# Performance work log

Hardware: AMD Instinct MI355X
Metric: run time of the kernel (lower is better)

The kernel has to match this reference:

```python
import jax, jax.numpy as jnp
import numpy as np
import math

NP2 = 64      # number of RF pulses
V = 32768     # number of voxels


def _shift_matrix(kmax):
    """EPG shift matrix, exact translation of EPG_shift_matrices."""
    N = 3 * (kmax + 1)
    S = np.zeros(N * N, dtype=np.complex64)
    kidx = list(range(3, N, 3)); sidx = [x - 3 for x in kidx]
    S[[a + N * b for a, b in zip(kidx, sidx)]] = 1
    kidx = list(range(4, N, 3)); kidx.pop(); sidx = [x + 3 for x in kidx]
    S[[a + N * b for a, b in zip(kidx, sidx)]] = 1
    kidx = list(range(2, N, 3))
    S[[a + N * b for a, b in zip(kidx, kidx)]] = 1
    S = S.reshape(N, N).T.copy()
    S[0:2, 4] = 1
    return jnp.asarray(S, dtype=jnp.complex64)


def _rf_rot_all(theta):
    """RF rotation matrices for all pulses at once. theta: [P] complex -> [P,3,3]."""
    a = jnp.abs(theta)
    phi = jnp.angle(theta)
    ca2 = (jnp.cos(a / 2) ** 2).astype(jnp.complex64)
    sa2 = jnp.sin(a / 2) ** 2
    sa = jnp.sin(a)
    ca = jnp.cos(a).astype(jnp.complex64)
    ep = jnp.exp(1j * phi)
    em = jnp.exp(-1j * phi)
    e2m = jnp.exp(-2j * phi)
    r00 = ca2
    r10 = e2m * sa2
    r20 = -0.5j * em * sa
    r01 = jnp.conj(r10)
    r11 = ca2
    r21 = 0.5j * ep * sa
    r02 = -1j * ep * sa
    r12 = 1j * em * sa
    r22 = ca
    row0 = jnp.stack([r00, r01, r02], axis=-1)
    row1 = jnp.stack([r10, r11, r12], axis=-1)
    row2 = jnp.stack([r20, r21, r22], axis=-1)
    return jnp.stack([row0, row1, row2], axis=-2).astype(jnp.complex64)


def _epg_gre_f0(theta, T1, T2, TR):
    """Single-compartment GRE EPG recurrence. Returns F0 signal [V, np2].

    Uses full-width (kmax) state updates every pulse: states beyond
    kmax_per_pulse are exactly zero on the ramp-up and cannot influence
    F0 on the ramp-down, so F0 matches the variable-width torch loop.
    """
    np2 = theta.shape[0]
    kmax = np2 - 1
    kpp_max = math.ceil(np2 / 2)
    if kpp_max < kmax:
        kmax = kpp_max
    K = kmax + 1
    N = 3 * K
    v = T1.shape[0]

    St = _shift_matrix(kmax).T                      # [N,N], so S @ f == f @ St
    E1 = jnp.exp(-TR / T1)[:, 0]                    # [V]
    E2 = jnp.exp(-TR / T2)[:, 0]                    # [V]
    # diagonal of kron(I_K, diag(E2,E2,E1)) per voxel -> [V,N]
    e = jnp.tile(jnp.stack([E2, E2, E1], axis=1), (1, K)).astype(jnp.complex64)
    b = jnp.zeros((v, N), jnp.complex64).at[:, 2].set((1 - E1).astype(jnp.complex64))

    A_all = _rf_rot_all(theta)                      # [np2,3,3]
    FF0 = jnp.zeros((v, N), jnp.complex64).at[:, 2].set(1.0)

    def step(FF, A):
        # block-diag kron(I_K, A) applied to the state vector
        Fcol = jnp.einsum('ab,vkb->vka', A, FF.reshape(v, K, 3)).reshape(v, N)
        # relaxation * shift + recovery
        FFn = e * (Fcol @ St) + b
        FFn = FFn.at[:, 0].set(jnp.conj(FFn[:, 0]))
        return FFn, Fcol[:, 0]

    _, F0 = jax.lax.scan(step, FF0, A_all)          # F0: [np2, V]
    return F0.T                                     # [V, np2]


def setup_inputs() -> dict:
    key = jax.random.key(0)
    k1, k2, k3, k4, k5 = jax.random.split(key, 5)
    flip = jax.random.uniform(k1, (NP2,), minval=0.1, maxval=math.pi / 2)
    phase = jax.random.uniform(k2, (NP2,), minval=-math.pi, maxval=math.pi)
    theta_re = (flip * jnp.cos(phase)).astype(jnp.float32)
    theta_im = (flip * jnp.sin(phase)).astype(jnp.float32)
    PD = jax.random.uniform(k3, (V, 1), minval=0.2, maxval=1.0)
    T1 = jax.random.uniform(k4, (V, 1), minval=300.0, maxval=1500.0)
    T2 = jax.random.uniform(k5, (V, 1), minval=20.0, maxval=120.0)
    qmaps = jnp.stack([PD, T1, T2], axis=0).astype(jnp.float32)  # [3,V,1]
    TR = jnp.array([10.0], jnp.float32)
    return {"theta_re": theta_re, "theta_im": theta_im, "TR": TR,
            "quantitative_maps": qmaps}


def reference(theta_re, theta_im, TR, quantitative_maps):
    theta = (theta_re + 1j * theta_im).astype(jnp.complex64)
    PD = quantitative_maps[0]   # [V,1]
    T1 = quantitative_maps[1]   # [V,1]
    T2 = quantitative_maps[2]   # [V,1]
    s = _epg_gre_f0(theta, T1, T2, TR)   # [V, np2] complex
    return jnp.abs(s) * PD
```

## Files before the change

### kernel.cpp

```cpp
#include <hip/hip_runtime.h>
#include <math.h>


#define NP2 64
#define ROR1  0x121
#define ROR15 0x12F

typedef float v2f __attribute__((ext_vector_type(2)));
typedef float v8f __attribute__((ext_vector_type(8)));

template<int CTRL>
__device__ __forceinline__ float rowrot(float x) {
    return __int_as_float(
        __builtin_amdgcn_mov_dpp(__float_as_int(x), CTRL, 0xF, 0xF, true));
}
__device__ __forceinline__ v2f mk2(float a, float b) { v2f r; r.x = a; r.y = b; return r; }

#define PAIR(V, i)  __builtin_shufflevector((V), (V), (i), (i) + 1)
#define FMA2(a, b, c) __builtin_elementwise_fma((a), (b), (c))

__global__ void coef_kernel(const float* __restrict__ theta_re,
                            const float* __restrict__ theta_im,
                            float* __restrict__ cw)
{
    const int t = threadIdx.x;
    if (t < NP2) {
        const float tre = theta_re[t], tim = theta_im[t];
        const float a2 = tre * tre + tim * tim;
        const float inva = __frsqrt_rn(a2);
        const float a = a2 * inva;
        const float c = tre * inva, s = tim * inva;
        float cp = 1.f, sp = 0.f;
        if (t > 0) {
            const float ure = theta_re[t - 1], uim = theta_im[t - 1];
            const float ia = __frsqrt_rn(ure * ure + uim * uim);
            cp = ure * ia; sp = uim * ia;
        }
        const float cd = cp * c + sp * s;
        const float sd = sp * c - cp * s;
        float sa, ca;
        __sincosf(a, &sa, &ca);
        const float ca2 = 0.5f + 0.5f * ca;
        const float sa2 = 0.5f - 0.5f * ca;
        const float h = 0.5f * sa;
        float4* row = (float4*)(cw + t * 16);
        row[0] = make_float4(cd, cd, sd, sd);
        row[1] = make_float4(ca2, ca2, sa2, sa2);
        row[2] = make_float4(sa, sa, ca, ca);
        row[3] = make_float4(h, h, 0.f, 0.f);
    } else if (t < NP2 + 4) {
        ((float4*)(cw + NP2 * 16))[t - NP2] = make_float4(0.f, 0.f, 0.f, 0.f);
    }
}

__global__ __launch_bounds__(256, 8) void epg_kernel(
    const float* __restrict__ TRp,
    const float* __restrict__ qmaps,
    const float* __restrict__ cw,
    float* __restrict__ out, int V)
{
    const int t = threadIdx.x;
    const int sub = t & 15;
    const int vloc = t >> 4;
    const int v = blockIdx.x * 16 + vloc;

    __shared__ __align__(16) v2f bufc[16][65];

    const float T1 = qmaps[V + v];
    const float T2 = qmaps[2 * V + v];
    const float tr = TRp[0];
    const float E1 = __expf(-tr / T1);
    const float E2 = __expf(-tr / T2);
    const v2f pE1 = mk2(E1, E1);
    const v2f pE2 = mk2(E2, E2);
    const float rE1s = (sub == 0) ? (1.0f - E1) : 0.0f;

    v2f Pr = mk2(0.f, 0.f), Pi = Pr, Mr = Pr, Mi = Pr, Zr = Pr, Zi = Pr;
    if (sub == 0) Zr.x = 1.0f;

    const bool s0 = (sub == 0);
    const bool s15 = (sub == 15);

    v8f A0, A1, B0, B1;
    asm volatile("s_load_dwordx8 %0, %1, 0x0"  : "=s"(B0) : "s"(cw));
    asm volatile("s_load_dwordx8 %0, %1, 0x20" : "=s"(B1) : "s"(cw));
    asm volatile("s_waitcnt lgkmcnt(0)"
                 : "=s"(A0), "=s"(A1) : "0"(B0), "1"(B1));

#pragma unroll 1
    for (int p = 0; p < NP2; ++p) {
        const float* nx = cw + (p + 1) * 16;
        asm volatile("s_load_dwordx8 %0, %1, 0x0"  : "=s"(B0) : "s"(nx));
        asm volatile("s_load_dwordx8 %0, %1, 0x20" : "=s"(B1) : "s"(nx));

        const v2f Ccd  = PAIR(A0, 0), Csd  = PAIR(A0, 2);
        const v2f Cca2 = PAIR(A0, 4), Csa2 = PAIR(A0, 6);
        const v2f Csa  = PAIR(A1, 0), Cca  = PAIR(A1, 2), Ch = PAIR(A1, 4);

        const v2f ec = pE2 * Ccd, es = pE2 * Csd;
        const v2f hPr = FMA2(ec, Pr, -(es * Pi));
        const v2f hPi = FMA2(ec, Pi,  (es * Pr));
        const v2f hMr = FMA2(ec, Mr,  (es * Mi));
        const v2f hMi = FMA2(ec, Mi, -(es * Mr));
        v2f ezr = pE1 * Zr;
        const v2f ezi = pE1 * Zi;
        ezr.x += rE1s;

        const v2f szr = Csa * ezr, szi = Csa * ezi;
        const v2f nPr = FMA2(Cca2, hPr, FMA2(Csa2, hMr,  szi));
        const v2f nPi = FMA2(Cca2, hPi, FMA2(Csa2, hMi, -szr));
        const v2f nMr = FMA2(Csa2, hPr, FMA2(Cca2, hMr, -szi));
        const v2f nMi = FMA2(Csa2, hPi, FMA2(Cca2, hMi,  szr));
        const v2f d1 = hPi - hMi, d2 = hMr - hPr;
        const v2f nZr = FMA2(Ch, d1, Cca * ezr);
        const v2f nZi = FMA2(Ch, d2, Cca * ezi);

        if (s0) bufc[vloc][p] = mk2(nPr.x, nPi.x);

        Zr = nZr; Zi = nZi;

        const float rPrx = rowrot<ROR1>(nPr.x),  rPry = rowrot<ROR1>(nPr.y);
        const float rPix = rowrot<ROR1>(nPi.x),  rPiy = rowrot<ROR1>(nPi.y);
        const float rMrx = rowrot<ROR15>(nMr.x), rMry = rowrot<ROR15>(nMr.y);
        const float rMix = rowrot<ROR15>(nMi.x), rMiy = rowrot<ROR15>(nMi.y);
        Pr.y = s0 ?  rPrx : rPry;
        Pi.y = s0 ?  rPix : rPiy;
        Pr.x = s0 ?  rMrx : rPrx;
        Pi.x = s0 ? -rMix : rPix;
        Mr.x = s15 ? rMry : rMrx;
        Mi.x = s15 ? rMiy : rMix;
        Mr.y = s15 ? 0.f : rMry;
        Mi.y = s15 ? 0.f : rMiy;

        asm volatile("s_waitcnt lgkmcnt(0)"
                     : "=s"(A0), "=s"(A1) : "0"(B0), "1"(B1));
    }

    __syncthreads();
    const int r = t >> 4;
    const int c = (t & 15) * 4;
    const float PDr = qmaps[blockIdx.x * 16 + r];
    const v2f a = bufc[r][c],     b = bufc[r][c + 1];
    const v2f d = bufc[r][c + 2], e = bufc[r][c + 3];
    float4 val;
    val.x = sqrtf(a.x * a.x + a.y * a.y) * PDr;
    val.y = sqrtf(b.x * b.x + b.y * b.y) * PDr;
    val.z = sqrtf(d.x * d.x + d.y * d.y) * PDr;
    val.w = sqrtf(e.x * e.x + e.y * e.y) * PDr;
    ((float4*)out)[blockIdx.x * 256 + t] = val;
}

extern "C" void kernel_launch(void* const* d_in, const int* in_sizes, int n_in,
                              void* d_out, int out_size, void* d_ws, size_t ws_size,
                              hipStream_t stream) {
    const float* theta_re = (const float*)d_in[0];
    const float* theta_im = (const float*)d_in[1];
    const float* TRp      = (const float*)d_in[2];
    const float* qmaps    = (const float*)d_in[3];
    float* out = (float*)d_out;
    float* cw  = (float*)d_ws;
    const int V = in_sizes[3] / 3;
    coef_kernel<<<dim3(1), dim3(128), 0, stream>>>(theta_re, theta_im, cw);
    epg_kernel<<<dim3(V / 16), dim3(256), 0, stream>>>(TRp, qmaps, cw, out, V);
}
```

Baseline: 109.0 us.

## Process two voxels per thread group to interleave independent EPG recurrences

Each 16-lane group now carries two independent voxel state vectors and advances both per pulse, halving the grid size. The second chain supplies instruction-level parallelism to hide DPP and FMA latency on the serial recurrence. It also amortizes the per-pulse scalar coefficient loads and waitcnt over twice the work. The cost is more registers per thread, which may reduce occupancy, and fewer blocks in flight.

```diff
diff --git a/kernel.cpp b/kernel.cpp
--- a/kernel.cpp
+++ b/kernel.cpp
@@ -53,6 +53,42 @@
     }
 }
 
+struct St { v2f Pr, Pi, Mr, Mi, Zr, Zi; };
+
+__device__ __forceinline__ v2f step(St& S,
+    v2f Ccd, v2f Csd, v2f Cca2, v2f Csa2, v2f Csa, v2f Cca, v2f Ch,
+    v2f pE1, v2f pE2, v2f rec, bool s0, bool s15)
+{
+    const v2f ec = pE2 * Ccd, es = pE2 * Csd;
+    const v2f hPr = FMA2(ec, S.Pr, -(es * S.Pi));
+    const v2f hPi = FMA2(ec, S.Pi,  (es * S.Pr));
+    const v2f hMr = FMA2(ec, S.Mr,  (es * S.Mi));
+    const v2f hMi = FMA2(ec, S.Mi, -(es * S.Mr));
+    const v2f ezr = FMA2(pE1, S.Zr, rec);
+    const v2f ezi = pE1 * S.Zi;
+    const v2f szr = Csa * ezr, szi = Csa * ezi;
+    const v2f nPr = FMA2(Cca2, hPr, FMA2(Csa2, hMr,  szi));
+    const v2f nPi = FMA2(Cca2, hPi, FMA2(Csa2, hMi, -szr));
+    const v2f nMr = FMA2(Csa2, hPr, FMA2(Cca2, hMr, -szi));
+    const v2f nMi = FMA2(Csa2, hPi, FMA2(Cca2, hMi,  szr));
+    const v2f d1 = hPi - hMi, d2 = hMr - hPr;
+    S.Zr = FMA2(Ch, d1, Cca * ezr);
+    S.Zi = FMA2(Ch, d2, Cca * ezi);
+    const float rPrx = rowrot<ROR1>(nPr.x),  rPry = rowrot<ROR1>(nPr.y);
+    const float rPix = rowrot<ROR1>(nPi.x),  rPiy = rowrot<ROR1>(nPi.y);
+    const float rMrx = rowrot<ROR15>(nMr.x), rMry = rowrot<ROR15>(nMr.y);
+    const float rMix = rowrot<ROR15>(nMi.x), rMiy = rowrot<ROR15>(nMi.y);
+    S.Pr.y = s0 ?  rPrx : rPry;
+    S.Pi.y = s0 ?  rPix : rPiy;
+    S.Pr.x = s0 ?  rMrx : rPrx;
+    S.Pi.x = s0 ? -rMix : rPix;
+    S.Mr.x = s15 ? rMry : rMrx;
+    S.Mi.x = s15 ? rMiy : rMix;
+    S.Mr.y = s15 ? 0.f : rMry;
+    S.Mi.y = s15 ? 0.f : rMiy;
+    return mk2(nPr.x, nPi.x);
+}
+
 __global__ __launch_bounds__(256, 8) void epg_kernel(
     const float* __restrict__ TRp,
     const float* __restrict__ qmaps,
@@ -62,24 +98,27 @@
     const int t = threadIdx.x;
     const int sub = t & 15;
     const int vloc = t >> 4;
-    const int v = blockIdx.x * 16 + vloc;
+    const int vA = blockIdx.x * 32 + vloc;
+    const int vB = vA + 16;
 
-    __shared__ __align__(16) v2f bufc[16][65];
+    __shared__ __align__(16) v2f bufc[32][65];
 
-    const float T1 = qmaps[V + v];
-    const float T2 = qmaps[2 * V + v];
     const float tr = TRp[0];
-    const float E1 = __expf(-tr / T1);
-    const float E2 = __expf(-tr / T2);
-    const v2f pE1 = mk2(E1, E1);
-    const v2f pE2 = mk2(E2, E2);
-    const float rE1s = (sub == 0) ? (1.0f - E1) : 0.0f;
-
-    v2f Pr = mk2(0.f, 0.f), Pi = Pr, Mr = Pr, Mi = Pr, Zr = Pr, Zi = Pr;
-    if (sub == 0) Zr.x = 1.0f;
-
+    const float E1A = __expf(-tr / qmaps[V + vA]);
+    const float E2A = __expf(-tr / qmaps[2 * V + vA]);
+    const float E1B = __expf(-tr / qmaps[V + vB]);
+    const float E2B = __expf(-tr / qmaps[2 * V + vB]);
     const bool s0 = (sub == 0);
     const bool s15 = (sub == 15);
+    const v2f pE1A = mk2(E1A, E1A), pE2A = mk2(E2A, E2A);
+    const v2f pE1B = mk2(E1B, E1B), pE2B = mk2(E2B, E2B);
+    const v2f recA = mk2(s0 ? (1.f - E1A) : 0.f, 0.f);
+    const v2f recB = mk2(s0 ? (1.f - E1B) : 0.f, 0.f);
+
+    St A, B;
+    A.Pr = mk2(0.f, 0.f); A.Pi = A.Pr; A.Mr = A.Pr; A.Mi = A.Pr; A.Zr = A.Pr; A.Zi = A.Pr;
+    B = A;
+    if (s0) { A.Zr.x = 1.0f; B.Zr.x = 1.0f; }
 
     v8f A0, A1, B0, B1;
     asm volatile("s_load_dwordx8 %0, %1, 0x0"  : "=s"(B0) : "s"(cw));
@@ -97,57 +136,36 @@
         const v2f Cca2 = PAIR(A0, 4), Csa2 = PAIR(A0, 6);
         const v2f Csa  = PAIR(A1, 0), Cca  = PAIR(A1, 2), Ch = PAIR(A1, 4);
 
-        const v2f ec = pE2 * Ccd, es = pE2 * Csd;
-        const v2f hPr = FMA2(ec, Pr, -(es * Pi));
-        const v2f hPi = FMA2(ec, Pi,  (es * Pr));
-        const v2f hMr = FMA2(ec, Mr,  (es * Mi));
-        const v2f hMi = FMA2(ec, Mi, -(es * Mr));
-        v2f ezr = pE1 * Zr;
-        const v2f ezi = pE1 * Zi;
-        ezr.x += rE1s;
-
-        const v2f szr = Csa * ezr, szi = Csa * ezi;
-        const v2f nPr = FMA2(Cca2, hPr, FMA2(Csa2, hMr,  szi));
-        const v2f nPi = FMA2(Cca2, hPi, FMA2(Csa2, hMi, -szr));
-        const v2f nMr = FMA2(Csa2, hPr, FMA2(Cca2, hMr, -szi));
-        const v2f nMi = FMA2(Csa2, hPi, FMA2(Cca2, hMi,  szr));
-        const v2f d1 = hPi - hMi, d2 = hMr - hPr;
-        const v2f nZr = FMA2(Ch, d1, Cca * ezr);
-        const v2f nZi = FMA2(Ch, d2, Cca * ezi);
-
-        if (s0) bufc[vloc][p] = mk2(nPr.x, nPi.x);
-
-        Zr = nZr; Zi = nZi;
-
-        const float rPrx = rowrot<ROR1>(nPr.x),  rPry = rowrot<ROR1>(nPr.y);
-        const float rPix = rowrot<ROR1>(nPi.x),  rPiy = rowrot<ROR1>(nPi.y);
-        const float rMrx = rowrot<ROR15>(nMr.x), rMry = rowrot<ROR15>(nMr.y);
-        const float rMix = rowrot<ROR15>(nMi.x), rMiy = rowrot<ROR15>(nMi.y);
-        Pr.y = s0 ?  rPrx : rPry;
-        Pi.y = s0 ?  rPix : rPiy;
-        Pr.x = s0 ?  rMrx : rPrx;
-        Pi.x = s0 ? -rMix : rPix;
-        Mr.x = s15 ? rMry : rMrx;
-        Mi.x = s15 ? rMiy : rMix;
-        Mr.y = s15 ? 0.f : rMry;
-        Mi.y = s15 ? 0.f : rMiy;
+        const v2f f0a = step(A, Ccd, Csd, Cca2, Csa2, Csa, Cca, Ch,
+                             pE1A, pE2A, recA, s0, s15);
+        const v2f f0b = step(B, Ccd, Csd, Cca2, Csa2, Csa, Cca, Ch,
+                             pE1B, pE2B, recB, s0, s15);
+        if (s0) {
+            bufc[vloc][p] = f0a;
+            bufc[vloc + 16][p] = f0b;
+        }
 
         asm volatile("s_waitcnt lgkmcnt(0)"
                      : "=s"(A0), "=s"(A1) : "0"(B0), "1"(B1));
     }
 
     __syncthreads();
-    const int r = t >> 4;
-    const int c = (t & 15) * 4;
-    const float PDr = qmaps[blockIdx.x * 16 + r];
-    const v2f a = bufc[r][c],     b = bufc[r][c + 1];
-    const v2f d = bufc[r][c + 2], e = bufc[r][c + 3];
-    float4 val;
-    val.x = sqrtf(a.x * a.x + a.y * a.y) * PDr;
-    val.y = sqrtf(b.x * b.x + b.y * b.y) * PDr;
-    val.z = sqrtf(d.x * d.x + d.y * d.y) * PDr;
-    val.w = sqrtf(e.x * e.x + e.y * e.y) * PDr;
-    ((float4*)out)[blockIdx.x * 256 + t] = val;
+    float4* out4 = (float4*)out;
+#pragma unroll
+    for (int i = 0; i < 2; ++i) {
+        const int q = i * 256 + t;
+        const int r = q >> 4;
+        const int c = (q & 15) * 4;
+        const float PDr = qmaps[blockIdx.x * 32 + r];
+        const v2f a = bufc[r][c],     b = bufc[r][c + 1];
+        const v2f d = bufc[r][c + 2], e = bufc[r][c + 3];
+        float4 val;
+        val.x = sqrtf(a.x * a.x + a.y * a.y) * PDr;
+        val.y = sqrtf(b.x * b.x + b.y * b.y) * PDr;
+        val.z = sqrtf(d.x * d.x + d.y * d.y) * PDr;
+        val.w = sqrtf(e.x * e.x + e.y * e.y) * PDr;
+        out4[blockIdx.x * 512 + q] = val;
+    }
 }
 
 extern "C" void kernel_launch(void* const* d_in, const int* in_sizes, int n_in,
@@ -161,5 +179,5 @@
     float* cw  = (float*)d_ws;
     const int V = in_sizes[3] / 3;
     coef_kernel<<<dim3(1), dim3(128), 0, stream>>>(theta_re, theta_im, cw);
-    epg_kernel<<<dim3(V / 16), dim3(256), 0, stream>>>(TRp, qmaps, cw, out, V);
+    epg_kernel<<<dim3(V / 32), dim3(256), 0, stream>>>(TRp, qmaps, cw, out, V);
 }
```

New measurement: 108.6 us. About the same (-0.4%).
